# Kernel tuning notes

Hardware: AMD Instinct MI355X
Metric: run time of the kernel (lower is better)

The kernel has to match this reference:

```python
import jax, jax.numpy as jnp
import numpy as np

D_MODEL = 1024
NUM_HEADS = 16
HEAD_DIM = D_MODEL // NUM_HEADS  # 64
M_BITS = 32
B, N = 4, 2048


def setup_inputs() -> dict:
    key = jax.random.key(0)
    ks = jax.random.split(key, 6)
    s = 1.0 / np.sqrt(D_MODEL)
    se = 1.0 / np.sqrt(HEAD_DIM)
    return {
        "x": jax.random.normal(ks[0], (B, N, D_MODEL), dtype=jnp.float32),
        "Wq": jax.random.normal(ks[1], (D_MODEL, D_MODEL), dtype=jnp.float32) * s,
        "Wk": jax.random.normal(ks[2], (D_MODEL, D_MODEL), dtype=jnp.float32) * s,
        "Wv": jax.random.normal(ks[3], (D_MODEL, D_MODEL), dtype=jnp.float32) * s,
        # per-head witness (bit) encoders: project head_dim -> m_bits
        "W_enc": jax.random.normal(ks[4], (NUM_HEADS, HEAD_DIM, M_BITS), dtype=jnp.float32) * se,
        "Wo": jax.random.normal(ks[5], (D_MODEL, D_MODEL), dtype=jnp.float32) * s,
    }


def reference(x, Wq, Wk, Wv, W_enc, Wo):
    Bsz, Nq, _ = x.shape
    # QKV projections (nn.Linear, no bias): y = x @ W^T
    Q = x @ Wq.T
    K = x @ Wk.T  # self-attention: context = x
    V = x @ Wv.T
    # split heads: [B, N, H, hd]
    Qh = Q.reshape(Bsz, Nq, NUM_HEADS, HEAD_DIM)
    Kh = K.reshape(Bsz, Nq, NUM_HEADS, HEAD_DIM)
    Vh = V.reshape(Bsz, Nq, NUM_HEADS, HEAD_DIM)
    # witness encodings: soft-bit (tanh of random-hyperplane projections), m_bits << head_dim feature space
    q_enc = jnp.tanh(jnp.einsum("bnhd,hdm->bnhm", Qh, W_enc))
    k_enc = jnp.tanh(jnp.einsum("bnhd,hdm->bnhm", Kh, W_enc))
    # witness similarity scores over m_bits instead of full head_dim
    scale = 1.0 / np.sqrt(M_BITS)
    scores = jnp.einsum("bnhm,bkhm->bhnk", q_enc, k_enc) * scale  # [B,H,N,N]
    attn = jax.nn.softmax(scores, axis=-1)
    out = jnp.einsum("bhnk,bkhd->bnhd", attn, Vh).reshape(Bsz, Nq, D_MODEL)
    return out @ Wo.T
```

## Files before the change

### kernel.cpp

```cpp
#include <hip/hip_runtime.h>

typedef unsigned short u16;
typedef unsigned int u32;

typedef __bf16 bfrag __attribute__((ext_vector_type(8)));
typedef float f32x4 __attribute__((ext_vector_type(4)));
typedef float f32x16 __attribute__((ext_vector_type(16)));
typedef float f32x2 __attribute__((ext_vector_type(2)));

__device__ __forceinline__ float b2f(u16 h) {
    u32 u = ((u32)h) << 16;
    return __builtin_bit_cast(float, u);
}
__device__ __forceinline__ u16 f2b(float f) {
    u32 u = __builtin_bit_cast(u32, f);
    u += 0x7fffu + ((u >> 16) & 1u);
    return (u16)(u >> 16);
}
__device__ __forceinline__ u32 cvtpk(float lo, float hi) {
    u32 r;
    asm("v_cvt_pk_bf16_f32 %0, %1, %2" : "=v"(r) : "v"(lo), "v"(hi));
    return r;
}

#if defined(__has_builtin)
#if __has_builtin(__builtin_amdgcn_exp2f)
#define EXP2(x) __builtin_amdgcn_exp2f(x)
#endif
#endif
#ifndef EXP2
#define EXP2(x) exp2f(x)
#endif

#if defined(__has_builtin)
#if __has_builtin(__builtin_amdgcn_global_load_lds)
#define HAS_GLL 1
#endif
#endif
#ifndef HAS_GLL
#define HAS_GLL 0
#endif

#if HAS_GLL
typedef __attribute__((address_space(1))) const u32 as1_u32;
typedef __attribute__((address_space(3))) u32 as3_u32;
__device__ __forceinline__ void gl_lds16(const u16* g, u16* l) {
    __builtin_amdgcn_global_load_lds((as1_u32*)g, (as3_u32*)l, 16, 0, 0);
}
#endif

#if defined(__has_builtin)
#if __has_builtin(__builtin_amdgcn_permlane32_swap)
#define HAS_PLS 1
#endif
#endif
#ifndef HAS_PLS
#define HAS_PLS 0
#endif

__device__ __forceinline__ void plswap(u32 a, u32 b, u32& o0, u32& o1) {
#if HAS_PLS
    auto r = __builtin_amdgcn_permlane32_swap((int)a, (int)b, false, false);
    o0 = (u32)r[0];
    o1 = (u32)r[1];
#else
    int idx = ((int)(threadIdx.x & 63) ^ 32) << 2;
    u32 ca = (u32)__builtin_amdgcn_ds_bpermute(idx, (int)a);
    u32 cb = (u32)__builtin_amdgcn_ds_bpermute(idx, (int)b);
    bool hi = (threadIdx.x & 63) >= 32;
    o0 = hi ? cb : a;
    o1 = hi ? b : ca;
#endif
}

__device__ __forceinline__ void xcd_swizzle(int& bxn, int& bym) {
    int gx = gridDim.x;
    int nwg = gx * gridDim.y;
    int orig = blockIdx.x + gx * blockIdx.y;
    int nid = orig;
    if ((nwg & 7) == 0) {
        int cpx = nwg >> 3;
        nid = (orig & 7) * cpx + (orig >> 3);
    }
    bxn = nid % gx;
    bym = nid / gx;
}

#define BATCH 4
#define SEQ   2048
#define DM    1024
#define NH    16
#define HD    64
#define MB    32
#define STOK  (BATCH * SEQ)

#define QSCALE 0.25503524337503433f
#define TWOLOG2E 2.8853900817779268f

__device__ __forceinline__ void storeC(u16* C, size_t idx, float v)   { C[idx] = f2b(v); }
__device__ __forceinline__ void storeC(float* C, size_t idx, float v) { C[idx] = v; }

__global__ __launch_bounds__(256) void cvt3_f32_bf16(
    const float* __restrict__ a, const float* __restrict__ b,
    const float* __restrict__ c,
    u16* __restrict__ da, u16* __restrict__ db, u16* __restrict__ dc,
    int n8a, int n8bc)
{
    const int Ba = n8a / 256;
    const int Bbc = n8bc / 256;
    int bid = blockIdx.x;
    const float* s;
    u16* d;
    int i;
    if (bid < Ba)            { s = a; d = da; i = bid * 256 + threadIdx.x; }
    else if (bid < Ba + Bbc) { s = b; d = db; i = (bid - Ba) * 256 + threadIdx.x; }
    else                     { s = c; d = dc; i = (bid - Ba - Bbc) * 256 + threadIdx.x; }
    const float4* sp = (const float4*)s + (size_t)i * 2;
    float4 x = sp[0], y = sp[1];
    u16 t[8] = { f2b(x.x), f2b(x.y), f2b(x.z), f2b(x.w),
                 f2b(y.x), f2b(y.y), f2b(y.z), f2b(y.w) };
    ((uint4*)d)[i] = *(uint4*)t;
}

__global__ __launch_bounds__(256) void build_cqk(
    const float* __restrict__ Wq, const float* __restrict__ Wk,
    const float* __restrict__ Wenc, u16* __restrict__ CqkT)
{
    const int dblk = blockIdx.x;
    const int qk   = blockIdx.y >> 4;
    const int h    = blockIdx.y & 15;
    const float* W = qk ? Wk : Wq;
    __shared__ float we[64][32];
    const int tid = threadIdx.x;

    for (int p = 0; p < 8; ++p) {
        int idx = p * 256 + tid;
        we[idx >> 5][idx & 31] = Wenc[(size_t)h * (HD * MB) + idx];
    }
    __syncthreads();

    const int mh = tid >> 7;
    const int d  = dblk * 128 + (tid & 127);
    float acc[16] = {};
    for (int dh = 0; dh < 64; ++dh) {
        float w = W[(size_t)(h * 64 + dh) * DM + d];
        for (int m = 0; m < 16; ++m)
            acc[m] += w * we[dh][mh * 16 + m];
    }
    u16* dst = CqkT + (size_t)(qk * 512 + h * 32 + mh * 16) * DM + d;
    for (int m = 0; m < 16; ++m)
        dst[(size_t)m * DM] = f2b(acc[m]);
}

template <int TBM, typename TC>
__global__ __launch_bounds__(256) void gemm_bt(
    const u16* __restrict__ A, const u16* __restrict__ Bt, TC* __restrict__ C,
    int M, int Nc, int K)
{
    constexpr int FI = TBM / 32;
    __shared__ alignas(16) u16 As[TBM * 32];
    __shared__ alignas(16) u16 Bs[128 * 32];

    const int tid  = threadIdx.x;
    const int wave = tid >> 6;
    const int lane = tid & 63;
    const int quad = lane >> 4;
    const int lrow = lane & 15;
    int bxn, bym;
    xcd_swizzle(bxn, bym);
    const int bm = bym * TBM;
    const int bn = bxn * 128;
    const int wm = (wave & 1) * (TBM / 2);
    const int wn = (wave >> 1) * 64;

    f32x4 acc[FI][4] = {};

    for (int k0 = 0; k0 < K; k0 += 32) {
#if HAS_GLL
        for (int p = 0; p < TBM / 64; ++p) {
            int cbase = wave * TBM + p * 64;
            int cme   = cbase + lane;
            int row = cme >> 2, col = (cme & 3) * 8;
            gl_lds16(&A[(size_t)(bm + row) * K + k0 + col], &As[(size_t)cbase * 8]);
        }
        for (int p = 0; p < 2; ++p) {
            int cbase = wave * 128 + p * 64;
            int cme   = cbase + lane;
            int row = cme >> 2, col = (cme & 3) * 8;
            gl_lds16(&Bt[(size_t)(bn + row) * K + k0 + col], &Bs[(size_t)cbase * 8]);
        }
#else
        for (int p = 0; p < TBM / 64; ++p) {
            int idx = p * 256 + tid, row = idx >> 2, col = (idx & 3) * 8;
            *(uint4*)&As[row * 32 + col] = *(const uint4*)&A[(size_t)(bm + row) * K + k0 + col];
        }
        for (int p = 0; p < 2; ++p) {
            int idx = p * 256 + tid, row = idx >> 2, col = (idx & 3) * 8;
            *(uint4*)&Bs[row * 32 + col] = *(const uint4*)&Bt[(size_t)(bn + row) * K + k0 + col];
        }
#endif
        __syncthreads();

        bfrag af[FI], bfv[4];
        for (int i = 0; i < FI; ++i)
            af[i] = *(const bfrag*)&As[(wm + i * 16 + lrow) * 32 + quad * 8];
        for (int j = 0; j < 4; ++j)
            bfv[j] = *(const bfrag*)&Bs[(wn + j * 16 + lrow) * 32 + quad * 8];

        for (int i = 0; i < FI; ++i)
            for (int j = 0; j < 4; ++j)
                acc[i][j] = __builtin_amdgcn_mfma_f32_16x16x32_bf16(af[i], bfv[j], acc[i][j], 0, 0, 0);
        __syncthreads();
    }

    for (int i = 0; i < FI; ++i)
        for (int j = 0; j < 4; ++j)
            for (int r = 0; r < 4; ++r) {
                int row = bm + wm + i * 16 + quad * 4 + r;
                int col = bn + wn + j * 16 + lrow;
                storeC(C, (size_t)row * Nc + col, acc[i][j][r]);
            }
}

__global__ __launch_bounds__(256) void gemm_encv(
    const u16* __restrict__ A, const u16* __restrict__ Bt,
    u16* __restrict__ qe, u16* __restrict__ ke, u16* __restrict__ Vt)
{
    __shared__ alignas(16) u16 As[128 * 32];
    __shared__ alignas(16) u16 Bs[128 * 32];

    const int tid  = threadIdx.x;
    const int wave = tid >> 6;
    const int lane = tid & 63;
    const int quad = lane >> 4;
    const int lrow = lane & 15;
    int bxn, bym;
    xcd_swizzle(bxn, bym);
    const int bm = bym * 128;
    const int bn = bxn * 128;
    const int wm = (wave & 1) * 64;
    const int wn = (wave >> 1) * 64;

    f32x4 acc[4][4] = {};

    for (int k0 = 0; k0 < DM; k0 += 32) {
#if HAS_GLL
        for (int p = 0; p < 2; ++p) {
            int cbase = wave * 128 + p * 64;
            int cme   = cbase + lane;
            int row = cme >> 2, col = (cme & 3) * 8;
            gl_lds16(&A[(size_t)(bm + row) * DM + k0 + col], &As[(size_t)cbase * 8]);
            gl_lds16(&Bt[(size_t)(bn + row) * DM + k0 + col], &Bs[(size_t)cbase * 8]);
        }
#else
        for (int p = 0; p < 2; ++p) {
            int idx = p * 256 + tid, row = idx >> 2, col = (idx & 3) * 8;
            *(uint4*)&As[row * 32 + col] = *(const uint4*)&A[(size_t)(bm + row) * DM + k0 + col];
            *(uint4*)&Bs[row * 32 + col] = *(const uint4*)&Bt[(size_t)(bn + row) * DM + k0 + col];
        }
#endif
        __syncthreads();

        bfrag af[4], bfv[4];
        for (int i = 0; i < 4; ++i)
            af[i] = *(const bfrag*)&As[(wm + i * 16 + lrow) * 32 + quad * 8];
        for (int j = 0; j < 4; ++j)
            bfv[j] = *(const bfrag*)&Bs[(wn + j * 16 + lrow) * 32 + quad * 8];

        for (int i = 0; i < 4; ++i)
            for (int j = 0; j < 4; ++j)
                acc[i][j] = __builtin_amdgcn_mfma_f32_16x16x32_bf16(af[i], bfv[j], acc[i][j], 0, 0, 0);
        __syncthreads();
    }

    if (bn < 1024) {
        for (int i = 0; i < 4; ++i)
            for (int j = 0; j < 4; ++j) {
                int col = bn + wn + j * 16 + lrow;
                int hh = (col >> 5) & 15;
                int mm = col & 31;
                u16* dst = (col < 512) ? qe : ke;
                float qs = (col < 512) ? QSCALE : 1.0f;
                for (int r = 0; r < 4; ++r) {
                    int row = bm + wm + i * 16 + quad * 4 + r;
                    int bb = row >> 11, nn = row & 2047;
                    float e = EXP2(acc[i][j][r] * TWOLOG2E);
                    float t = (1.f - 2.f / (e + 1.f)) * qs;
                    dst[((size_t)(bb * NH + hh) * SEQ + nn) * MB + mm] = f2b(t);
                }
            }
    } else {
        for (int i = 0; i < 4; ++i)
            for (int j = 0; j < 4; ++j) {
                int col = bn - 1024 + wn + j * 16 + lrow;
                int hh = col >> 6, dd = col & 63;
                int row0 = bm + wm + i * 16 + quad * 4;
                int bb = row0 >> 11, nn = row0 & 2047;
                u16 t4[4] = { f2b(acc[i][j][0]), f2b(acc[i][j][1]),
                              f2b(acc[i][j][2]), f2b(acc[i][j][3]) };
                *(uint2*)&Vt[((size_t)(bb * NH + hh) * HD + dd) * SEQ + nn] = *(uint2*)t4;
            }
    }
}

__global__ __launch_bounds__(256, 4) void flash_attn(
    const u16* __restrict__ qe,
    const u16* __restrict__ ke,
    const u16* __restrict__ Vt,
    u16* __restrict__ AO)
{
    const int h = blockIdx.x, b = blockIdx.y, qt = blockIdx.z;
    const int tid  = threadIdx.x;
    const int wave = tid >> 6;
    const int lane = tid & 63;
    const int r31  = lane & 31;
    const int hi   = lane >> 5;

    __shared__ alignas(16) u16 Kt[2][64 * 32];
    __shared__ alignas(16) u16 Vtile[2][64 * 64];

    const size_t bhh = (size_t)(b * NH + h);
    const u16* keb = ke + bhh * SEQ * MB;
    const u16* qeb = qe + bhh * SEQ * MB;
    const u16* vtb = Vt + bhh * HD * SEQ;

    const int q0w = qt * 128 + wave * 32;

    const int klr = tid >> 2;
    const int ksl = tid & 3;
    const u16* ksrc = keb + (size_t)klr * MB + ((ksl ^ (klr & 3)) * 8);
    const int d0 = wave * 8 + (lane >> 3);
    const int c0 = lane & 7;
    const int g0 = (c0 ^ (d0 & 7)) * 8;
    const u16* vsrc0 = vtb + (size_t)d0 * SEQ + g0;
    const u16* vsrc1 = vtb + (size_t)(d0 + 32) * SEQ + g0;

#if HAS_GLL
    gl_lds16(ksrc,  Kt[0] + wave * 512);
    gl_lds16(vsrc0, Vtile[0] + wave * 512);
    gl_lds16(vsrc1, Vtile[0] + 2048 + wave * 512);
#else
    *(uint4*)&Kt[0][klr * 32 + ksl * 8] = *(const uint4*)ksrc;
    *(uint4*)&Vtile[0][d0 * 64 + c0 * 8] = *(const uint4*)vsrc0;
    *(uint4*)&Vtile[0][(d0 + 32) * 64 + c0 * 8] = *(const uint4*)vsrc1;
#endif
    ksrc += 64 * MB;
    vsrc0 += 64;
    vsrc1 += 64;

    bfrag qf[2];
    {
        const u16* qrow = qeb + (size_t)(q0w + r31) * MB;
        qf[0] = *(const bfrag*)&qrow[hi * 8];
        qf[1] = *(const bfrag*)&qrow[16 + hi * 8];
    }

    const f32x16 zero16 = {};

    f32x16 Oa[2] = {};
    f32x2 dacc = {0.f, 0.f};
    const int ksw = r31 & 3;
    const int vsw = r31 & 7;

    for (int c = 0; c < 32; ++c) {
        const int cur = c & 1, nxt = cur ^ 1;
        __syncthreads();

        if (c + 1 < 32) {
#if HAS_GLL
            gl_lds16(ksrc,  Kt[nxt] + wave * 512);
            gl_lds16(vsrc0, Vtile[nxt] + wave * 512);
            gl_lds16(vsrc1, Vtile[nxt] + 2048 + wave * 512);
#else
            *(uint4*)&Kt[nxt][klr * 32 + ksl * 8] = *(const uint4*)ksrc;
            *(uint4*)&Vtile[nxt][d0 * 64 + c0 * 8] = *(const uint4*)vsrc0;
            *(uint4*)&Vtile[nxt][(d0 + 32) * 64 + c0 * 8] = *(const uint4*)vsrc1;
#endif
            ksrc += 64 * MB;
            vsrc0 += 64;
            vsrc1 += 64;
        }

        const u16* KtC = Kt[cur];
        const u16* VtC = Vtile[cur];

        bfrag kf[2][2];
        for (int kt = 0; kt < 2; ++kt) {
            const u16* krow = &KtC[(kt * 32 + r31) * 32];
            kf[kt][0] = *(const bfrag*)&krow[((hi    ) ^ ksw) * 8];
            kf[kt][1] = *(const bfrag*)&krow[((2 + hi) ^ ksw) * 8];
        }

        bfrag pf[2][2];
        for (int kt = 0; kt < 2; ++kt) {
            __builtin_amdgcn_s_setprio(1);
            f32x16 St = __builtin_amdgcn_mfma_f32_32x32x16_bf16(kf[kt][0], qf[0], zero16, 0, 0, 0);
            St = __builtin_amdgcn_mfma_f32_32x32x16_bf16(kf[kt][1], qf[1], St, 0, 0, 0);
            __builtin_amdgcn_s_setprio(0);
            for (int kc = 0; kc < 2; ++kc) {
                float e0 = EXP2(St[8 * kc + 0]);
                float e1 = EXP2(St[8 * kc + 1]);
                float e2 = EXP2(St[8 * kc + 2]);
                float e3 = EXP2(St[8 * kc + 3]);
                float e4 = EXP2(St[8 * kc + 4]);
                float e5 = EXP2(St[8 * kc + 5]);
                float e6 = EXP2(St[8 * kc + 6]);
                float e7 = EXP2(St[8 * kc + 7]);
                f32x2 p0 = {e0, e1}, p1 = {e2, e3}, p2 = {e4, e5}, p3 = {e6, e7};
                dacc += (p0 + p1) + (p2 + p3);
                u32 A0 = cvtpk(e0, e1), A1 = cvtpk(e2, e3);
                u32 B0 = cvtpk(e4, e5), B1 = cvtpk(e6, e7);
                u32 w0, w1, w2, w3;
                plswap(A0, B0, w0, w2);
                plswap(A1, B1, w1, w3);
                uint4 words = { w0, w1, w2, w3 };
                pf[kt][kc] = __builtin_bit_cast(bfrag, words);
            }
        }

        __builtin_amdgcn_s_setprio(1);
        for (int dt = 0; dt < 2; ++dt) {
            const u16* vrow = &VtC[(dt * 32 + r31) * 64];
            for (int kt = 0; kt < 2; ++kt)
                for (int kc = 0; kc < 2; ++kc) {
                    bfrag vf = *(const bfrag*)&vrow[(((kt * 4 + kc * 2 + hi) ^ vsw) * 8)];
                    Oa[dt] = __builtin_amdgcn_mfma_f32_32x32x16_bf16(vf, pf[kt][kc], Oa[dt], 0, 0, 0);
                }
        }
        __builtin_amdgcn_s_setprio(0);
    }

    float dsum = dacc[0] + dacc[1];
    u32 o0, o1;
    plswap(__builtin_bit_cast(u32, dsum), __builtin_bit_cast(u32, dsum), o0, o1);
    float den = __builtin_bit_cast(float, o0) + __builtin_bit_cast(float, o1);

    {
        float inv = 1.0f / den;
        u16* aob = AO + (size_t)(b * SEQ + q0w + r31) * DM + h * HD;
        for (int dt = 0; dt < 2; ++dt)
            for (int g = 0; g < 4; ++g) {
                u16 t4[4] = { f2b(Oa[dt][g * 4 + 0] * inv),
                              f2b(Oa[dt][g * 4 + 1] * inv),
                              f2b(Oa[dt][g * 4 + 2] * inv),
                              f2b(Oa[dt][g * 4 + 3] * inv) };
                *(uint2*)&aob[dt * 32 + g * 8 + hi * 4] = *(uint2*)t4;
            }
    }
}

extern "C" void kernel_launch(void* const* d_in, const int* in_sizes, int n_in,
                              void* d_out, int out_size, void* d_ws, size_t ws_size,
                              hipStream_t stream) {
    const float* x    = (const float*)d_in[0];
    const float* Wq   = (const float*)d_in[1];
    const float* Wk   = (const float*)d_in[2];
    const float* Wv   = (const float*)d_in[3];
    const float* Wenc = (const float*)d_in[4];
    const float* Wo   = (const float*)d_in[5];
    float* out = (float*)d_out;

    const size_t MB1 = (size_t)1024 * 1024;
    char* ws = (char*)d_ws;
    u16* AO   = (u16*)(ws);
    u16* Wo_b = (u16*)(ws + 16 * MB1);
    u16* Bc   = (u16*)(ws + 18 * MB1);
    u16* Vt   = (u16*)(ws + 24 * MB1);
    u16* qe   = (u16*)(ws + 48 * MB1);
    u16* ke   = (u16*)(ws + 56 * MB1);

    u16* xb = (u16*)d_out;
    u16* wvb = Bc + (size_t)1024 * DM;

    const int n8a = STOK * DM / 8;
    const int n8bc = DM * DM / 8;
    cvt3_f32_bf16<<<dim3(n8a / 256 + 2 * (n8bc / 256)), 256, 0, stream>>>(
        x, Wv, Wo, xb, wvb, Wo_b, n8a, n8bc);
    build_cqk<<<dim3(8, 32), 256, 0, stream>>>(Wq, Wk, Wenc, Bc);

    gemm_encv<<<dim3(2048 / 128, STOK / 128), 256, 0, stream>>>(xb, Bc, qe, ke, Vt);

    flash_attn<<<dim3(NH, BATCH, SEQ / 128), 256, 0, stream>>>(qe, ke, Vt, AO);

    gemm_bt<64, float><<<dim3(DM / 128, STOK / 64), 256, 0, stream>>>(AO, Wo_b, out, STOK, DM, DM);
}
```

Baseline: 253.1 us.

## Merge conversion and Cqk build kernels; halve gemm_encv M tile

Folds the f32-to-bf16 conversion kernel and the build_cqk kernel into one launch, with the block index choosing which job each block does. This removes one kernel launch and the serialization between the two. It also cuts the gemm_encv tile from 128 to 64 rows, doubling the grid to 4096 blocks to raise occupancy and balance across CUs. The cost is less operand reuse per block and more redundant B-tile loads.

```diff
diff --git a/kernel.cpp b/kernel.cpp
--- a/kernel.cpp
+++ b/kernel.cpp
@@ -100,38 +100,39 @@
 __device__ __forceinline__ void storeC(u16* C, size_t idx, float v)   { C[idx] = f2b(v); }
 __device__ __forceinline__ void storeC(float* C, size_t idx, float v) { C[idx] = v; }
 
-__global__ __launch_bounds__(256) void cvt3_f32_bf16(
-    const float* __restrict__ a, const float* __restrict__ b,
-    const float* __restrict__ c,
-    u16* __restrict__ da, u16* __restrict__ db, u16* __restrict__ dc,
-    int n8a, int n8bc)
+__global__ __launch_bounds__(256) void prep(
+    const float* __restrict__ x, const float* __restrict__ Wv,
+    const float* __restrict__ Wo, const float* __restrict__ Wq,
+    const float* __restrict__ Wk, const float* __restrict__ Wenc,
+    u16* __restrict__ xb, u16* __restrict__ wvb, u16* __restrict__ wob,
+    u16* __restrict__ CqkT, int n8a, int n8bc)
 {
-    const int Ba = n8a / 256;
-    const int Bbc = n8bc / 256;
-    int bid = blockIdx.x;
-    const float* s;
-    u16* d;
-    int i;
-    if (bid < Ba)            { s = a; d = da; i = bid * 256 + threadIdx.x; }
-    else if (bid < Ba + Bbc) { s = b; d = db; i = (bid - Ba) * 256 + threadIdx.x; }
-    else                     { s = c; d = dc; i = (bid - Ba - Bbc) * 256 + threadIdx.x; }
-    const float4* sp = (const float4*)s + (size_t)i * 2;
-    float4 x = sp[0], y = sp[1];
-    u16 t[8] = { f2b(x.x), f2b(x.y), f2b(x.z), f2b(x.w),
-                 f2b(y.x), f2b(y.y), f2b(y.z), f2b(y.w) };
-    ((uint4*)d)[i] = *(uint4*)t;
-}
-
-__global__ __launch_bounds__(256) void build_cqk(
-    const float* __restrict__ Wq, const float* __restrict__ Wk,
-    const float* __restrict__ Wenc, u16* __restrict__ CqkT)
-{
-    const int dblk = blockIdx.x;
-    const int qk   = blockIdx.y >> 4;
-    const int h    = blockIdx.y & 15;
+    const int Ba = n8a / 256, Bbc = n8bc / 256;
+    const int bid = blockIdx.x;
+    const int tid = threadIdx.x;
+    __shared__ float we[64][32];
+
+    if (bid < Ba + 2 * Bbc) {
+        const float* s;
+        u16* d;
+        int i;
+        if (bid < Ba)            { s = x;  d = xb;  i = bid * 256 + tid; }
+        else if (bid < Ba + Bbc) { s = Wv; d = wvb; i = (bid - Ba) * 256 + tid; }
+        else                     { s = Wo; d = wob; i = (bid - Ba - Bbc) * 256 + tid; }
+        const float4* sp = (const float4*)s + (size_t)i * 2;
+        float4 a = sp[0], y = sp[1];
+        u16 t[8] = { f2b(a.x), f2b(a.y), f2b(a.z), f2b(a.w),
+                     f2b(y.x), f2b(y.y), f2b(y.z), f2b(y.w) };
+        ((uint4*)d)[i] = *(uint4*)t;
+        return;
+    }
+
+    const int bid2 = bid - Ba - 2 * Bbc;
+    const int dblk = bid2 & 7;
+    const int yid  = bid2 >> 3;
+    const int qk   = yid >> 4;
+    const int h    = yid & 15;
     const float* W = qk ? Wk : Wq;
-    __shared__ float we[64][32];
-    const int tid = threadIdx.x;
 
     for (int p = 0; p < 8; ++p) {
         int idx = p * 256 + tid;
@@ -226,7 +227,7 @@
     const u16* __restrict__ A, const u16* __restrict__ Bt,
     u16* __restrict__ qe, u16* __restrict__ ke, u16* __restrict__ Vt)
 {
-    __shared__ alignas(16) u16 As[128 * 32];
+    __shared__ alignas(16) u16 As[64 * 32];
     __shared__ alignas(16) u16 Bs[128 * 32];
 
     const int tid  = threadIdx.x;
@@ -236,45 +237,53 @@
     const int lrow = lane & 15;
     int bxn, bym;
     xcd_swizzle(bxn, bym);
-    const int bm = bym * 128;
+    const int bm = bym * 64;
     const int bn = bxn * 128;
-    const int wm = (wave & 1) * 64;
+    const int wm = (wave & 1) * 32;
     const int wn = (wave >> 1) * 64;
 
-    f32x4 acc[4][4] = {};
+    f32x4 acc[2][4] = {};
 
     for (int k0 = 0; k0 < DM; k0 += 32) {
 #if HAS_GLL
+        {
+            int cbase = wave * 64;
+            int cme   = cbase + lane;
+            int row = cme >> 2, col = (cme & 3) * 8;
+            gl_lds16(&A[(size_t)(bm + row) * DM + k0 + col], &As[(size_t)cbase * 8]);
+        }
         for (int p = 0; p < 2; ++p) {
             int cbase = wave * 128 + p * 64;
             int cme   = cbase + lane;
             int row = cme >> 2, col = (cme & 3) * 8;
-            gl_lds16(&A[(size_t)(bm + row) * DM + k0 + col], &As[(size_t)cbase * 8]);
             gl_lds16(&Bt[(size_t)(bn + row) * DM + k0 + col], &Bs[(size_t)cbase * 8]);
         }
 #else
+        {
+            int idx = tid, row = idx >> 2, col = (idx & 3) * 8;
+            *(uint4*)&As[row * 32 + col] = *(const uint4*)&A[(size_t)(bm + row) * DM + k0 + col];
+        }
         for (int p = 0; p < 2; ++p) {
             int idx = p * 256 + tid, row = idx >> 2, col = (idx & 3) * 8;
-            *(uint4*)&As[row * 32 + col] = *(const uint4*)&A[(size_t)(bm + row) * DM + k0 + col];
             *(uint4*)&Bs[row * 32 + col] = *(const uint4*)&Bt[(size_t)(bn + row) * DM + k0 + col];
         }
 #endif
         __syncthreads();
 
-        bfrag af[4], bfv[4];
-        for (int i = 0; i < 4; ++i)
+        bfrag af[2], bfv[4];
+        for (int i = 0; i < 2; ++i)
             af[i] = *(const bfrag*)&As[(wm + i * 16 + lrow) * 32 + quad * 8];
         for (int j = 0; j < 4; ++j)
             bfv[j] = *(const bfrag*)&Bs[(wn + j * 16 + lrow) * 32 + quad * 8];
 
-        for (int i = 0; i < 4; ++i)
+        for (int i = 0; i < 2; ++i)
             for (int j = 0; j < 4; ++j)
                 acc[i][j] = __builtin_amdgcn_mfma_f32_16x16x32_bf16(af[i], bfv[j], acc[i][j], 0, 0, 0);
         __syncthreads();
     }
 
     if (bn < 1024) {
-        for (int i = 0; i < 4; ++i)
+        for (int i = 0; i < 2; ++i)
             for (int j = 0; j < 4; ++j) {
                 int col = bn + wn + j * 16 + lrow;
                 int hh = (col >> 5) & 15;
@@ -290,7 +299,7 @@
                 }
             }
     } else {
-        for (int i = 0; i < 4; ++i)
+        for (int i = 0; i < 2; ++i)
             for (int j = 0; j < 4; ++j) {
                 int col = bn - 1024 + wn + j * 16 + lrow;
                 int hh = col >> 6, dd = col & 63;
@@ -474,11 +483,10 @@
 
     const int n8a = STOK * DM / 8;
     const int n8bc = DM * DM / 8;
-    cvt3_f32_bf16<<<dim3(n8a / 256 + 2 * (n8bc / 256)), 256, 0, stream>>>(
-        x, Wv, Wo, xb, wvb, Wo_b, n8a, n8bc);
-    build_cqk<<<dim3(8, 32), 256, 0, stream>>>(Wq, Wk, Wenc, Bc);
-
-    gemm_encv<<<dim3(2048 / 128, STOK / 128), 256, 0, stream>>>(xb, Bc, qe, ke, Vt);
+    prep<<<dim3(n8a / 256 + 2 * (n8bc / 256) + 256), 256, 0, stream>>>(
+        x, Wv, Wo, Wq, Wk, Wenc, xb, wvb, Wo_b, Bc, n8a, n8bc);
+
+    gemm_encv<<<dim3(2048 / 128, STOK / 64), 256, 0, stream>>>(xb, Bc, qe, ke, Vt);
 
     flash_attn<<<dim3(NH, BATCH, SEQ / 128), 256, 0, stream>>>(qe, ke, Vt, AO);
 
```

Result: no change. 256.9 us (+1.5%).
